# Performance work log

Measured on AMD Instinct MI355X. Metric: run time of the kernel, lower is better.

## Reference

```python
import jax, jax.numpy as jnp
import numpy as np

H = 2048
W = 2048

# 2x2 derivative kernels (classic Lucas-Kanade / Horn-Schunck estimates)
_KX = np.array([[-1.0, 1.0], [-1.0, 1.0]], dtype=np.float32) * 0.25
_KY = np.array([[-1.0, -1.0], [1.0, 1.0]], dtype=np.float32) * 0.25
_KT = np.array([[1.0, 1.0], [1.0, 1.0]], dtype=np.float32) * 0.25


def _conv2d(x, k, padding):
    # x: (H, W), k: (kh, kw) -> (H', W')
    return jax.lax.conv_general_dilated(
        x[None, None], k[None, None].astype(x.dtype), (1, 1), padding
    )[0, 0]


def _deriv(img, k):
    # replicate-pad bottom/right so the 2x2 valid conv returns (H, W)
    p = jnp.pad(img, ((0, 1), (0, 1)), mode='edge')
    return _conv2d(p, jnp.asarray(k), 'VALID')


def setup_inputs() -> dict:
    key = jax.random.key(0)
    k1, k2 = jax.random.split(key)
    image_prev = jax.random.uniform(k1, (1, 1, H, W), dtype=jnp.float32)
    image_next = jax.random.uniform(k2, (1, 1, H, W), dtype=jnp.float32)
    return {"image_prev": image_prev, "image_next": image_next, "window_size": 15}


def reference(image_prev, image_next, window_size):
    prev = image_prev[0, 0]  # (H, W); original code only uses batch 0, channel 0
    nxt = image_next[0, 0]

    fx = 0.5 * (_deriv(prev, _KX) + _deriv(nxt, _KX))
    fy = 0.5 * (_deriv(prev, _KY) + _deriv(nxt, _KY))
    ft = _deriv(nxt, _KT) - _deriv(prev, _KT)

    w = int(window_size)
    ones = jnp.ones((w, w), dtype=fx.dtype)

    def box(f):
        # window sum with zero padding == ZeroPad2d(n) + w x w sliding sum
        return _conv2d(f, ones, 'SAME')

    Axx = box(fx * fx)
    Axy = box(fx * fy)
    Ayy = box(fy * fy)
    bx = box(fx * ft)
    by = box(fy * ft)

    det = Axx * Ayy - Axy * Axy
    valid = det != 0
    safe_det = jnp.where(valid, det, jnp.ones_like(det))
    # [[Axx,Axy],[Axy,Ayy]]^{-1} @ [bx, by]
    u = jnp.where(valid, (Ayy * bx - Axy * by) / safe_det, 0.0)
    v = jnp.where(valid, (Axx * by - Axy * bx) / safe_det, 0.0)

    return jnp.stack([u, v])[None]  # (1, 2, H, W)
```

## Files before the change

kernel.cpp:

```cpp
#include <hip/hip_runtime.h>


constexpr int IH  = 2048;
constexpr int IW  = 2048;
constexpr int RAD = 7;
constexpr int WIN = 15;
constexpr int NT  = 64;
constexpr int SW  = 112;
constexpr int RB  = 8;
constexpr int SCAN = RB + WIN - 1;
constexpr int NSTRIP = 19;
constexpr int NBAND  = IH / RB;
constexpr int NXCD   = 8;
constexpr int CHUNK  = NBAND / NXCD;

struct Row { float sp0, sp1, dt0, dt1; };

template<bool YE>
__device__ __forceinline__ Row load_row(const float* __restrict__ P,
                                        const float* __restrict__ N,
                                        int row, int pcb, bool lload) {
    if constexpr (YE) row = row < 0 ? 0 : (row > IH - 1 ? IH - 1 : row);
    float2 q = make_float2(0.f, 0.f), r = q;
    if (lload) {
        const size_t off = (size_t)row * IW + pcb;
        q = *reinterpret_cast<const float2*>(P + off);
        r = *reinterpret_cast<const float2*>(N + off);
    }
    Row R;
    R.sp0 = q.x + r.x; R.dt0 = r.x - q.x;
    R.sp1 = q.y + r.y; R.dt1 = r.y - q.y;
    return R;
}

template<bool SUB, bool XE>
__device__ __forceinline__ void accum(float V[5][2], const Row& A, const Row& B,
                                      int t, bool ok, bool rep2) {
    const float g0 = A.sp0 + B.sp0, g1 = A.sp1 + B.sp1;
    const float m0 = B.sp0 - A.sp0, m1 = B.sp1 - A.sp1;
    const float e0 = A.dt0 + B.dt0, e1 = A.dt1 + B.dt1;
    float g2 = __shfl(g0, t + 1);
    float m2 = __shfl(m0, t + 1);
    float e2 = __shfl(e0, t + 1);
    if constexpr (XE) {
        g2 = rep2 ? g1 : g2; m2 = rep2 ? m1 : m2; e2 = rep2 ? e1 : e2;
    }
    float fx0 = g1 - g0, fy0 = m0 + m1, ft0 = e0 + e1;
    float fx1 = g2 - g1, fy1 = m1 + m2, ft1 = e1 + e2;
    if constexpr (XE) {
        fx0 = ok ? fx0 : 0.f; fy0 = ok ? fy0 : 0.f; ft0 = ok ? ft0 : 0.f;
        fx1 = ok ? fx1 : 0.f; fy1 = ok ? fy1 : 0.f; ft1 = ok ? ft1 : 0.f;
    }
    if constexpr (!SUB) {
        V[0][0] += fx0 * fx0; V[1][0] += fx0 * fy0; V[2][0] += fy0 * fy0;
        V[3][0] += fx0 * ft0; V[4][0] += fy0 * ft0;
        V[0][1] += fx1 * fx1; V[1][1] += fx1 * fy1; V[2][1] += fy1 * fy1;
        V[3][1] += fx1 * ft1; V[4][1] += fy1 * ft1;
    } else {
        V[0][0] -= fx0 * fx0; V[1][0] -= fx0 * fy0; V[2][0] -= fy0 * fy0;
        V[3][0] -= fx0 * ft0; V[4][0] -= fy0 * ft0;
        V[0][1] -= fx1 * fx1; V[1][1] -= fx1 * fy1; V[2][1] -= fy1 * fy1;
        V[3][1] -= fx1 * ft1; V[4][1] -= fy1 * ft1;
    }
}

template<bool XE, bool YE>
__device__ __forceinline__ void lk_body(const float* __restrict__ P,
                                        const float* __restrict__ N,
                                        float* __restrict__ out,
                                        int c0, int r0, int t) {
    const int pcb = c0 - 8 + 2 * t;
    bool ok = true, rep2 = false;
    if constexpr (XE) {
        ok   = ((unsigned)pcb < (unsigned)IW);
        rep2 = (pcb + 2 >= IW) && ok;
    }
    const bool lload = ok;

    float V[5][2] = {};

    Row E0 = load_row<YE>(P, N, r0 - 7, pcb, lload);
    Row E1 = load_row<YE>(P, N, r0 - 6, pcb, lload);
    Row E2 = load_row<YE>(P, N, r0 - 5, pcb, lload);
    Row E3 = load_row<YE>(P, N, r0 - 4, pcb, lload);
    Row E4 = load_row<YE>(P, N, r0 - 3, pcb, lload);
    Row E5 = load_row<YE>(P, N, r0 - 2, pcb, lload);
    Row X0, X1, X2, X3, X4;

    #pragma unroll
    for (int sr = 0; sr < SCAN; ++sr) {
        const int pr = r0 - RAD + sr;

        Row nE, nX;
        const bool doE = (sr <= 16);
        if (doE) nE = load_row<YE>(P, N, pr + 6, pcb, lload);
        const bool doX = (sr >= 10 && sr <= 17);
        if (doX) nX = load_row<YE>(P, N, r0 + sr - 17, pcb, lload);

        bool enter_ok = true;
        if constexpr (YE) enter_ok = (pr >= 0) && (pr < IH);
        if (enter_ok) accum<false, XE>(V, E0, E1, t, ok, rep2);

        if (sr >= WIN) {
            bool exit_ok = true;
            if constexpr (YE) exit_ok = (pr - WIN) >= 0;
            if (exit_ok) accum<true, XE>(V, X0, X1, t, ok, rep2);
        }

        if (sr >= WIN - 1) {
            float a0[5], a1[5];
            #pragma unroll
            for (int p = 0; p < 5; ++p) {
                const float Pg = V[p][0] + V[p][1];
                float S = Pg + __shfl(Pg, t + 1);
                S += __shfl(S, t + 2);
                S += __shfl(S, t + 4);
                const float q0 = __shfl(V[p][0], t + 8);
                a0[p] = S - V[p][0];
                a1[p] = (S - Pg) + q0;
            }
            const float det0 = a0[0] * a0[2] - a0[1] * a0[1];
            const float rd0  = __builtin_amdgcn_rcpf(det0) * 2.0f;
            const bool  k0   = (det0 != 0.f);
            const float det1 = a1[0] * a1[2] - a1[1] * a1[1];
            const float rd1  = __builtin_amdgcn_rcpf(det1) * 2.0f;
            const bool  k1   = (det1 != 0.f);
            float2 qu, qv;
            qu.x = k0 ? (a0[2] * a0[3] - a0[1] * a0[4]) * rd0 : 0.f;
            qv.x = k0 ? (a0[0] * a0[4] - a0[1] * a0[3]) * rd0 : 0.f;
            qu.y = k1 ? (a1[2] * a1[3] - a1[1] * a1[4]) * rd1 : 0.f;
            qv.y = k1 ? (a1[0] * a1[4] - a1[1] * a1[3]) * rd1 : 0.f;

            const int i  = r0 + sr - (WIN - 1);
            const int x0 = c0 + 2 * t;
            if ((2 * t < SW) && (x0 < IW)) {
                *reinterpret_cast<float2*>(out + (size_t)i * IW + x0) = qu;
                *reinterpret_cast<float2*>(out + (size_t)IH * IW + (size_t)i * IW + x0) = qv;
            }
        }

        E0 = E1; E1 = E2; E2 = E3; E3 = E4; E4 = E5; if (doE) E5 = nE;
        if (sr == 10)      X0 = nX;
        else if (sr == 11) X1 = nX;
        else if (sr == 12) X2 = nX;
        else if (sr == 13) X3 = nX;
        else if (sr == 14) X4 = nX;
        else if (sr >= 15) { X0 = X1; X1 = X2; X2 = X3; X3 = X4; if (sr <= 17) X4 = nX; }
    }
}

__global__ __launch_bounds__(NT)
void lk_kernel(const float* __restrict__ Pimg, const float* __restrict__ Nimg,
               float* __restrict__ out) {
    const int bid   = blockIdx.x;
    const int xcd   = bid & 7;
    const int idx   = bid >> 3;
    const int strip = idx / CHUNK;
    const int pos   = idx % CHUNK;
    const int band  = xcd * CHUNK + pos;
    const int c0 = strip * SW;
    const int r0 = band * RB;
    const int t  = threadIdx.x;
    const bool xe = (strip == 0) || (strip == NSTRIP - 1);
    const bool ye = (band == 0) || (band == NBAND - 1);
    if (!xe && !ye)      lk_body<false, false>(Pimg, Nimg, out, c0, r0, t);
    else if (xe && !ye)  lk_body<true,  false>(Pimg, Nimg, out, c0, r0, t);
    else if (!xe)        lk_body<false, true >(Pimg, Nimg, out, c0, r0, t);
    else                 lk_body<true,  true >(Pimg, Nimg, out, c0, r0, t);
}

extern "C" void kernel_launch(void* const* d_in, const int* in_sizes, int n_in,
                              void* d_out, int out_size, void* d_ws, size_t ws_size,
                              hipStream_t stream) {
    (void)in_sizes; (void)n_in; (void)d_ws; (void)ws_size; (void)out_size;
    const float* prev = (const float*)d_in[0];
    const float* nxt  = (const float*)d_in[1];
    float* out        = (float*)d_out;
    dim3 grid(NSTRIP * NBAND);
    dim3 block(NT);
    hipLaunchKernelGGL(lk_kernel, grid, block, 0, stream, prev, nxt, out);
}
```

Baseline: 31.26 us.

## Double row band height and reuse entered rows via LDS ring instead of reloading

Each block now processes 16 output rows instead of 8, which halves the number of blocks and the share of halo rows loaded per output row. Rows leaving the sliding window are no longer reloaded from global memory; the entering row data is written to a 16-slot shared-memory ring per thread and read back 14 iterations later. This trades global/L2 reloads for LDS traffic and a longer unrolled loop, and fewer blocks means less parallelism on the GPU.

```diff
diff --git a/kernel.cpp b/kernel.cpp
--- a/kernel.cpp
+++ b/kernel.cpp
@@ -7,12 +7,13 @@
 constexpr int WIN = 15;
 constexpr int NT  = 64;
 constexpr int SW  = 112;
-constexpr int RB  = 8;
+constexpr int RB  = 16;
 constexpr int SCAN = RB + WIN - 1;
 constexpr int NSTRIP = 19;
 constexpr int NBAND  = IH / RB;
 constexpr int NXCD   = 8;
 constexpr int CHUNK  = NBAND / NXCD;
+constexpr int RING   = 16;
 
 struct Row { float sp0, sp1, dt0, dt1; };
 
@@ -68,6 +69,7 @@
 __device__ __forceinline__ void lk_body(const float* __restrict__ P,
                                         const float* __restrict__ N,
                                         float* __restrict__ out,
+                                        float4* __restrict__ ring,
                                         int c0, int r0, int t) {
     const int pcb = c0 - 8 + 2 * t;
     bool ok = true, rep2 = false;
@@ -85,17 +87,22 @@
     Row E3 = load_row<YE>(P, N, r0 - 4, pcb, lload);
     Row E4 = load_row<YE>(P, N, r0 - 3, pcb, lload);
     Row E5 = load_row<YE>(P, N, r0 - 2, pcb, lload);
-    Row X0, X1, X2, X3, X4;
+    Row XA, XB;
 
     #pragma unroll
     for (int sr = 0; sr < SCAN; ++sr) {
         const int pr = r0 - RAD + sr;
 
-        Row nE, nX;
-        const bool doE = (sr <= 16);
+        Row nE;
+        const bool doE = (sr <= 24);
         if (doE) nE = load_row<YE>(P, N, pr + 6, pcb, lload);
-        const bool doX = (sr >= 10 && sr <= 17);
-        if (doX) nX = load_row<YE>(P, N, r0 + sr - 17, pcb, lload);
+
+        ring[(sr & 15) * NT + t] = make_float4(E0.sp0, E0.sp1, E0.dt0, E0.dt1);
+        if (sr >= 14) {
+            XA = XB;
+            const float4 rr = ring[((sr - 14) & 15) * NT + t];
+            XB.sp0 = rr.x; XB.sp1 = rr.y; XB.dt0 = rr.z; XB.dt1 = rr.w;
+        }
 
         bool enter_ok = true;
         if constexpr (YE) enter_ok = (pr >= 0) && (pr < IH);
@@ -104,7 +111,7 @@
         if (sr >= WIN) {
             bool exit_ok = true;
             if constexpr (YE) exit_ok = (pr - WIN) >= 0;
-            if (exit_ok) accum<true, XE>(V, X0, X1, t, ok, rep2);
+            if (exit_ok) accum<true, XE>(V, XA, XB, t, ok, rep2);
         }
 
         if (sr >= WIN - 1) {
@@ -140,18 +147,14 @@
         }
 
         E0 = E1; E1 = E2; E2 = E3; E3 = E4; E4 = E5; if (doE) E5 = nE;
-        if (sr == 10)      X0 = nX;
-        else if (sr == 11) X1 = nX;
-        else if (sr == 12) X2 = nX;
-        else if (sr == 13) X3 = nX;
-        else if (sr == 14) X4 = nX;
-        else if (sr >= 15) { X0 = X1; X1 = X2; X2 = X3; X3 = X4; if (sr <= 17) X4 = nX; }
     }
 }
 
 __global__ __launch_bounds__(NT)
 void lk_kernel(const float* __restrict__ Pimg, const float* __restrict__ Nimg,
                float* __restrict__ out) {
+    __shared__ float4 ring[RING * NT];
+
     const int bid   = blockIdx.x;
     const int xcd   = bid & 7;
     const int idx   = bid >> 3;
@@ -163,10 +166,10 @@
     const int t  = threadIdx.x;
     const bool xe = (strip == 0) || (strip == NSTRIP - 1);
     const bool ye = (band == 0) || (band == NBAND - 1);
-    if (!xe && !ye)      lk_body<false, false>(Pimg, Nimg, out, c0, r0, t);
-    else if (xe && !ye)  lk_body<true,  false>(Pimg, Nimg, out, c0, r0, t);
-    else if (!xe)        lk_body<false, true >(Pimg, Nimg, out, c0, r0, t);
-    else                 lk_body<true,  true >(Pimg, Nimg, out, c0, r0, t);
+    if (!xe && !ye)      lk_body<false, false>(Pimg, Nimg, out, ring, c0, r0, t);
+    else if (xe && !ye)  lk_body<true,  false>(Pimg, Nimg, out, ring, c0, r0, t);
+    else if (!xe)        lk_body<false, true >(Pimg, Nimg, out, ring, c0, r0, t);
+    else                 lk_body<true,  true >(Pimg, Nimg, out, ring, c0, r0, t);
 }
 
 extern "C" void kernel_launch(void* const* d_in, const int* in_sizes, int n_in,
```

Measured after the change: 34.21 us. 9.4% more time.
